# Kernel optimization log

Hardware: AMD Instinct MI355X
Metric: run time of the kernel (lower is better)

## Reference

```python
import jax, jax.numpy as jnp
import numpy as np
from jax import lax

HID = 128
NGRAPH = 64  # ligands per receptor


def _conv3d(x, w, b):
    # x: [N,C,D,H,W], w: [O,I,3,3,3], VALID padding (torch Conv3d default)
    y = lax.conv_general_dilated(x, w, (1, 1, 1), 'VALID',
                                 dimension_numbers=('NCDHW', 'OIDHW', 'NCDHW'))
    return y + b[None, :, None, None, None]


def setup_inputs() -> dict:
    key = jax.random.key(0)
    ks = jax.random.split(key, 40)
    i = iter(range(40))
    rn = lambda shape, s=1.0: jax.random.normal(ks[next(i)], shape, jnp.float32) * s
    W = 0.02
    inp = {
        'ms_feat_0': rn((4, 32, 16, 16, 16)),
        'ms_feat_1': rn((4, 64, 8, 8, 8)),
        'token_features': rn((4, 128, 256)),
        'lig_atom': rn((4, 1024, 64)),
        'lig_graph': rn((4, NGRAPH, 64)),
        'ligand_batch': jnp.sort(jax.random.randint(ks[next(i)], (1024,), 0, NGRAPH)).astype(jnp.int32),
        # token_mlp
        'W_token': rn((256, HID), W), 'b_token': jnp.zeros((HID,)),
        # pocket_mlp_list (reversed order: conv0 <- ms_feat_1 C=64, conv1 <- ms_feat_0 C=32)
        'Wc0': rn((HID, 64, 3, 3, 3), W), 'bc0': jnp.zeros((HID,)),
        'Wc1': rn((HID, 32, 3, 3, 3), W), 'bc1': jnp.zeros((HID,)),
        # pocket_mlp
        'W_pocket': rn((2 * HID, HID), W), 'b_pocket': jnp.zeros((HID,)),
        # concat layer / gate
        'W_cat': rn((3 * HID, HID), W), 'b_cat': jnp.zeros((HID,)),
        'W_gate': rn((3 * HID, HID), W), 'b_gate': jnp.zeros((HID,)),
        # ligand projections
        'W_atom': rn((64, HID), W), 'b_atom': jnp.zeros((HID,)),
        'W_graph': rn((64, HID), W), 'b_graph': jnp.zeros((HID,)),
        # energy bias mlp
        'W_bias1': rn((2 * HID, HID), W), 'b_bias1': jnp.zeros((HID,)),
        'W_bias2': rn((HID, 1), W), 'b_bias2': jnp.zeros((1,)),
        # interaction mlp + pair energy / gate
        'W_int': rn((HID, HID), W), 'b_int': jnp.zeros((HID,)),
        'W_pe': rn((HID, 1), W), 'b_pe': jnp.zeros((1,)),
        'W_pg': rn((HID, 1), W), 'b_pg': jnp.zeros((1,)),
    }
    return inp


def reference(ms_feat_0, ms_feat_1, token_features, lig_atom, lig_graph, ligand_batch,
              W_token, b_token, Wc0, bc0, Wc1, bc1, W_pocket, b_pocket,
              W_cat, b_cat, W_gate, b_gate, W_atom, b_atom, W_graph, b_graph,
              W_bias1, b_bias1, W_bias2, b_bias2, W_int, b_int,
              W_pe, b_pe, W_pg, b_pg):
    silu = jax.nn.silu
    lrelu = lambda x: jax.nn.leaky_relu(x, 0.01)

    # ---- ready_to_calculate ----
    # reversed multi-scale: [ms_feat_1, ms_feat_0]; SiLU -> Conv3d -> spatial mean
    p0 = _conv3d(silu(ms_feat_1), Wc0, bc0).mean(axis=(2, 3, 4))  # [N,HID]
    p1 = _conv3d(silu(ms_feat_0), Wc1, bc1).mean(axis=(2, 3, 4))  # [N,HID]
    pocket = silu(jnp.concatenate([p0, p1], -1)) @ W_pocket + b_pocket  # [N,HID]

    tok = silu(token_features) @ W_token + b_token                # [N,Nt,HID]
    tok_agg = jnp.concatenate([tok.sum(1), tok.mean(1)], -1)      # [N,2*HID]

    pf = jnp.concatenate([pocket, tok_agg], -1)                   # [N,3*HID]
    pf = (pf @ W_cat + b_cat) * jax.nn.sigmoid(pf @ W_gate + b_gate)  # [N,HID]

    # ---- per-image affinity (vectorized over images) ----
    atoms = lig_atom @ W_atom + b_atom                            # [N,Na,HID]
    # einsum('ik,jk->ijk') outer interaction map, batched over images
    imap = jnp.einsum('nik,njk->nijk', atoms, tok)                # [N,Na,Nt,HID]
    h = lrelu(imap @ W_int + b_int)                               # [N,Na,Nt,HID]
    pe = (h @ W_pe + b_pe) * jax.nn.sigmoid(h @ W_pg + b_pg)      # [N,Na,Nt,1]
    atom_e = pe.sum(axis=(2, 3))                                  # [N,Na]
    seg = jax.vmap(lambda v: jax.ops.segment_sum(v, ligand_batch, num_segments=NGRAPH))(atom_e)  # [N,Ng]

    gf = lig_graph @ W_graph + b_graph                            # [N,Ng,HID]
    pf_rep = jnp.broadcast_to(pf[:, None, :], gf.shape)           # [N,Ng,HID]
    z = jnp.concatenate([pf_rep, gf], -1)                         # [N,Ng,2*HID]
    bias = lrelu(z @ W_bias1 + b_bias1) @ W_bias2 + b_bias2       # [N,Ng,1]

    return seg + bias[..., 0]                                     # [N,Ng]
```

## Files before the change

### kernel.cpp

```cpp
#include <hip/hip_runtime.h>
#include <hip/hip_bf16.h>

#define NIMG 4

typedef __attribute__((ext_vector_type(8))) _Float16 half8v;
typedef __attribute__((ext_vector_type(2))) _Float16 half2v;
typedef __attribute__((ext_vector_type(4))) float float4v;
typedef __attribute__((ext_vector_type(4))) int   int4v;

__device__ __forceinline__ float sigm(float x){ return 1.f/(1.f+__expf(-x)); }
__device__ __forceinline__ float silu(float x){ return x/(1.f+__expf(-x)); }
__device__ __forceinline__ float lrelu(float x){ return fmaxf(x, 0.01f*x); }

template<int CTRL>
__device__ __forceinline__ float dpp_radd(float v){
  int s = __builtin_amdgcn_update_dpp(0, __builtin_bit_cast(int, v), CTRL, 0xF, 0xF, true);
  return v + __builtin_bit_cast(float, s);
}
__device__ __forceinline__ float row16_reduce(float v){
  v = dpp_radd<0x128>(v);
  v = dpp_radd<0x124>(v);
  v = dpp_radd<0x122>(v);
  v = dpp_radd<0x121>(v);
  return v;
}

__device__ __forceinline__ half8v scale_frag16(half8v a, const int* tpk){
  int4v ai = __builtin_bit_cast(int4v, a);
  int4v oi;
  #pragma unroll
  for(int p=0;p<4;p++){
    int r;
    asm("v_pk_mul_f16 %0, %1, %2" : "=v"(r) : "v"(ai[p]), "v"(tpk[p]));
    oi[p] = r;
  }
  return __builtin_bit_cast(half8v, oi);
}

template<int DIM, int ODIM>
__device__ void wsum_body(const float* __restrict__ x, float* __restrict__ S,
                          int vb, float* sh){
  const float* xp = x + (size_t)vb*(DIM*DIM*DIM);
  for(int p=threadIdx.x; p<DIM*DIM*DIM; p+=256) sh[p] = silu(xp[p]);
  __syncthreads();
  const int wave = threadIdx.x>>6, lane = threadIdx.x&63;
  for(int tap=wave; tap<27; tap+=4){
    const int kd=tap/9, kh=(tap/3)%3, kw=tap%3;
    const int base = kd*DIM*DIM + kh*DIM + kw;
    float ps = 0.f;
    for(int idx=lane; idx<ODIM*ODIM*ODIM; idx+=64){
      int od = idx/(ODIM*ODIM); int r = idx - od*(ODIM*ODIM);
      int oh = r/ODIM; int ow = r - oh*ODIM;
      ps += sh[base + od*DIM*DIM + oh*DIM + ow];
    }
    #pragma unroll
    for(int m=32;m>=1;m>>=1) ps += __shfl_xor(ps,m);
    if(lane==0) S[vb*27 + tap] = ps;
  }
}

__global__ __launch_bounds__(256) void k_pre(
    const float* __restrict__ tf, const float* __restrict__ Wtok,
    const float* __restrict__ btok, float* __restrict__ tok,
    const float* __restrict__ ms1, float* __restrict__ S1,
    const float* __restrict__ ms0, float* __restrict__ S0,
    const float* __restrict__ la, const float* __restrict__ Wa,
    const float* __restrict__ ba, unsigned short* __restrict__ atoms_h,
    float* __restrict__ atom_e,
    const float* __restrict__ Wint, unsigned short* __restrict__ Wt){
  __shared__ float sh[4096];
  const int b = blockIdx.x;
  const int tid = threadIdx.x;
  if(b < 512){
    const int row = b;
    sh[tid] = silu(tf[row*256 + tid]);
    __syncthreads();
    const int c = tid & 127, sg = tid >> 7;
    float acc = 0.f;
    #pragma unroll 8
    for(int q=sg*128; q<sg*128+128; q++) acc = fmaf(sh[q], Wtok[q*128+c], acc);
    if(sg==1) sh[256+c] = acc;
    __syncthreads();
    if(sg==0) tok[row*128+c] = acc + sh[256+c] + btok[c];
  } else if(b < 768){
    wsum_body<8,6>(ms1, S1, b-512, sh);
  } else if(b < 896){
    wsum_body<16,14>(ms0, S0, b-768, sh);
  } else if(b < 2944){
    const int rowb = (b-896)*2;
    if(tid < 128) sh[tid] = la[(size_t)rowb*64 + tid];
    __syncthreads();
    const int r2 = tid>>7, c = tid&127;
    const float* s = sh + r2*64;
    float acc = ba[c];
    #pragma unroll 8
    for(int k=0;k<64;k++) acc = fmaf(s[k], Wa[k*128+c], acc);
    atoms_h[(size_t)(rowb+r2)*128 + c] = __builtin_bit_cast(unsigned short, (_Float16)acc);
    if(tid<2) atom_e[rowb+tid] = 0.f;
  } else {
    const int idx = (b-2944)*256 + tid;
    const int c = idx >> 7, k = idx & 127;
    Wt[c*128 + k] = __builtin_bit_cast(unsigned short, (_Float16)(Wint[k*128 + c]));
  }
}

__global__ void k_pconv(const float* __restrict__ S1, const float* __restrict__ S0,
                        const float* __restrict__ Wc0, const float* __restrict__ bc0,
                        const float* __restrict__ Wc1, const float* __restrict__ bc1,
                        const float* __restrict__ tok, float* __restrict__ toksum,
                        float* __restrict__ pp){
  const int b = blockIdx.x;
  const int n = b >> 7, c = b & 127;
  const int tid = threadIdx.x;
  float a0 = 0.f, a1 = 0.f, ts = 0.f;
  { const float* w = Wc0 + c*1728; const float* s = S1 + n*1728;
    for(int q=tid; q<1728; q+=256) a0 = fmaf(w[q], s[q], a0); }
  { const float* w = Wc1 + c*864;  const float* s = S0 + n*864;
    for(int q=tid; q<864; q+=256)  a1 = fmaf(w[q], s[q], a1); }
  for(int j=tid; j<128; j+=256) ts = tok[(n*128+j)*128 + c];
  #pragma unroll
  for(int m=32;m>=1;m>>=1){
    a0 += __shfl_xor(a0,m); a1 += __shfl_xor(a1,m); ts += __shfl_xor(ts,m);
  }
  __shared__ float r0[4], r1[4], r2[4];
  if((tid&63)==0){ r0[tid>>6]=a0; r1[tid>>6]=a1; r2[tid>>6]=ts; }
  __syncthreads();
  if(tid==0){
    float p0 = bc0[c] + (r0[0]+r0[1]+r0[2]+r0[3])*(1.f/216.f);
    float p1 = bc1[c] + (r1[0]+r1[1]+r1[2]+r1[3])*(1.f/2744.f);
    pp[n*256 + c]       = silu(p0);
    pp[n*256 + 128 + c] = silu(p1);
    toksum[n*128 + c]   = r2[0]+r2[1]+r2[2]+r2[3];
  }
}

__global__ void k_pf2(const float* __restrict__ pp, const float* __restrict__ toksum,
                      const float* __restrict__ Wp,  const float* __restrict__ bp,
                      const float* __restrict__ Wcat, const float* __restrict__ bcat,
                      const float* __restrict__ Wgate,const float* __restrict__ bgate,
                      float* __restrict__ pf){
  __shared__ float ps[256];
  __shared__ float zz[384];
  __shared__ float part[4][128];
  __shared__ float partg[4][128];
  const int n = blockIdx.x;
  const int tid = threadIdx.x;
  const int c = tid & 127, s = tid >> 7;
  if(tid < 256) ps[tid] = pp[n*256 + tid];
  __syncthreads();
  float a = 0.f;
  for(int q=s*64; q<s*64+64; q++) a = fmaf(ps[q], Wp[q*128+c], a);
  part[s][c] = a;
  __syncthreads();
  if(s==0){
    float pk = bp[c] + part[0][c]+part[1][c]+part[2][c]+part[3][c];
    float ts = toksum[n*128+c];
    zz[c] = pk; zz[128+c] = ts; zz[256+c] = ts*(1.f/128.f);
  }
  __syncthreads();
  float a1=0.f, a2=0.f;
  for(int q=s*96; q<s*96+96; q++){
    float z = zz[q];
    a1 = fmaf(z, Wcat[q*128+c], a1);
    a2 = fmaf(z, Wgate[q*128+c], a2);
  }
  part[s][c]=a1; partg[s][c]=a2;
  __syncthreads();
  if(s==0){
    float v1 = bcat[c] +part[0][c]+part[1][c]+part[2][c]+part[3][c];
    float v2 = bgate[c]+partg[0][c]+partg[1][c]+partg[2][c]+partg[3][c];
    pf[n*128+c] = v1 * sigm(v2);
  }
}

__global__ __launch_bounds__(256,2) void k_inter(
    const unsigned short* __restrict__ atoms_h,
    const float* __restrict__ tok,
    const unsigned short* __restrict__ Wt,
    const float* __restrict__ bint,
    const float* __restrict__ Wpe, const float* __restrict__ bpe,
    const float* __restrict__ Wpg, const float* __restrict__ bpg,
    float* __restrict__ atom_e){
  __shared__ float red[8][2][2][32][2];

  const int b0 = blockIdx.x;
  const int bid = (b0 & 7)*128 + (b0 >> 3);
  const int n = bid >> 8;
  const int chunk = (bid >> 4) & 15;
  const int jg = bid & 15;
  const int tid = threadIdx.x;
  const int w = tid >> 6, lane = tid & 63;
  const int t = lane & 15, q = lane >> 4;
  const int g = w >> 1, wc = w & 1;

  const int rbase = n*1024 + chunk*64;

  half8v areg[2][4];
  { const unsigned short* ab = atoms_h + (size_t)(rbase + g*32 + t)*128 + q*8;
    #pragma unroll
    for(int fr=0;fr<2;fr++)
      #pragma unroll
      for(int ks=0;ks<4;ks++)
        areg[fr][ks] = *(const half8v*)(ab + fr*16*128 + ks*32);
  }
  half8v breg[4][4];
  { const unsigned short* wb = Wt + (size_t)(wc*64 + t)*128 + q*8;
    #pragma unroll
    for(int fc=0;fc<4;fc++)
      #pragma unroll
      for(int ks=0;ks<4;ks++)
        breg[fc][ks] = *(const half8v*)(wb + fc*16*128 + ks*32);
  }
  float bi[4], wpe[4], wpg[4];
  #pragma unroll
  for(int fc=0;fc<4;fc++){
    int cc = wc*64 + fc*16 + t;
    bi[fc]=bint[cc]; wpe[fc]=Wpe[cc]; wpg[fc]=Wpg[cc];
  }
  const float bpe0 = bpe[0], bpg0 = bpg[0];
  const float* tokn = tok + (size_t)(n*128 + jg*8)*128 + q*8;

  #pragma unroll
  for(int j=0;j<8;j++){
    int tpk[4][4];
    { const float* tr = tokn + j*128;
      #pragma unroll
      for(int ks=0;ks<4;ks++){
        float4v t0 = *(const float4v*)(tr + ks*32);
        float4v t1 = *(const float4v*)(tr + ks*32 + 4);
        tpk[ks][0] = __builtin_bit_cast(int, __builtin_amdgcn_cvt_pkrtz(t0[0],t0[1]));
        tpk[ks][1] = __builtin_bit_cast(int, __builtin_amdgcn_cvt_pkrtz(t0[2],t0[3]));
        tpk[ks][2] = __builtin_bit_cast(int, __builtin_amdgcn_cvt_pkrtz(t1[0],t1[1]));
        tpk[ks][3] = __builtin_bit_cast(int, __builtin_amdgcn_cvt_pkrtz(t1[2],t1[3]));
      }
    }
    float4v acc[2][4];
    #pragma unroll
    for(int fr=0;fr<2;fr++)
      #pragma unroll
      for(int fc=0;fc<4;fc++)
        acc[fr][fc] = (float4v){bi[fc],bi[fc],bi[fc],bi[fc]};
    #pragma unroll
    for(int ks=0;ks<4;ks++){
      half8v s0 = scale_frag16(areg[0][ks], tpk[ks]);
      half8v s1 = scale_frag16(areg[1][ks], tpk[ks]);
      #pragma unroll
      for(int fc=0;fc<4;fc++){
        acc[0][fc] = __builtin_amdgcn_mfma_f32_16x16x32_f16(s0, breg[fc][ks], acc[0][fc], 0,0,0);
        acc[1][fc] = __builtin_amdgcn_mfma_f32_16x16x32_f16(s1, breg[fc][ks], acc[1][fc], 0,0,0);
      }
    }
    #pragma unroll
    for(int fr=0;fr<2;fr++){
      #pragma unroll
      for(int r=0;r<4;r++){
        float d1=0.f, d2=0.f;
        #pragma unroll
        for(int fc=0;fc<4;fc++){
          float h = lrelu(acc[fr][fc][r]);
          d1 = fmaf(h, wpe[fc], d1);
          d2 = fmaf(h, wpg[fc], d2);
        }
        d1 = row16_reduce(d1);
        d2 = row16_reduce(d2);
        if(t==0){
          int a = fr*16 + q*4 + r;
          red[j][g][wc][a][0] = d1;
          red[j][g][wc][a][1] = d2;
        }
      }
    }
  }
  __syncthreads();
  if(tid < 64){
    const int gg = tid >> 5, a = tid & 31;
    float s_ = 0.f;
    #pragma unroll
    for(int j=0;j<8;j++){
      float d1 = red[j][gg][0][a][0] + red[j][gg][1][a][0];
      float d2 = red[j][gg][0][a][1] + red[j][gg][1][a][1];
      s_ += (d1 + bpe0) * sigm(d2 + bpg0);
    }
    atomicAdd(atom_e + rbase + tid, s_);
  }
}

__global__ __launch_bounds__(256) void k_bias_seg(
    const float* __restrict__ lg, const float* __restrict__ Wg,
    const float* __restrict__ bg, const float* __restrict__ pf,
    const float* __restrict__ W1, const float* __restrict__ b1,
    const float* __restrict__ W2, const float* __restrict__ b2,
    const float* __restrict__ atom_e, const int* __restrict__ batch,
    float* __restrict__ out){
  __shared__ float row[64];
  __shared__ float z[256];
  __shared__ float partA[128];
  __shared__ float partB[128];
  __shared__ float wred[4];
  const int b = blockIdx.x;
  const int n = b >> 6, g = b & 63;
  const int tid = threadIdx.x;
  const int c = tid & 127, s = tid >> 7;
  if(tid < 64) row[tid] = lg[b*64 + tid];
  __syncthreads();
  float gf = 0.f;
  #pragma unroll 8
  for(int k=s*32;k<s*32+32;k++) gf = fmaf(row[k], Wg[k*128+c], gf);
  if(s==1) partA[c] = gf;
  __syncthreads();
  if(s==0){ z[c] = pf[n*128+c]; z[128+c] = gf + partA[c] + bg[c]; }
  __syncthreads();
  float tacc = 0.f;
  for(int qq=s*128; qq<s*128+128; qq++) tacc = fmaf(z[qq], W1[qq*128+c], tacc);
  if(s==1) partB[c] = tacc;
  float se = 0.f;
  const float* ae = atom_e + n*1024;
  for(int i=tid;i<1024;i+=256){ float v = ae[i]; se += (batch[i]==g) ? v : 0.f; }
  __syncthreads();
  float val = se;
  if(s==0){
    float tf = lrelu(tacc + partB[c] + b1[c]);
    val += tf * W2[c];
  }
  #pragma unroll
  for(int m=32;m>=1;m>>=1) val += __shfl_xor(val,m);
  if((tid&63)==0) wred[tid>>6] = val;
  __syncthreads();
  if(tid==0) out[b] = wred[0]+wred[1]+wred[2]+wred[3] + b2[0];
}

extern "C" void kernel_launch(void* const* d_in, const int* in_sizes, int n_in,
                              void* d_out, int out_size, void* d_ws, size_t ws_size,
                              hipStream_t stream) {
  const float* ms0   = (const float*)d_in[0];
  const float* ms1   = (const float*)d_in[1];
  const float* tfeat = (const float*)d_in[2];
  const float* la    = (const float*)d_in[3];
  const float* lg    = (const float*)d_in[4];
  const int*   batch = (const int*)  d_in[5];
  const float* Wtok  = (const float*)d_in[6];
  const float* btok  = (const float*)d_in[7];
  const float* Wc0   = (const float*)d_in[8];
  const float* bc0   = (const float*)d_in[9];
  const float* Wc1   = (const float*)d_in[10];
  const float* bc1   = (const float*)d_in[11];
  const float* Wp    = (const float*)d_in[12];
  const float* bp    = (const float*)d_in[13];
  const float* Wcat  = (const float*)d_in[14];
  const float* bcat  = (const float*)d_in[15];
  const float* Wgate = (const float*)d_in[16];
  const float* bgate = (const float*)d_in[17];
  const float* Wa    = (const float*)d_in[18];
  const float* ba    = (const float*)d_in[19];
  const float* Wgr   = (const float*)d_in[20];
  const float* bgr   = (const float*)d_in[21];
  const float* W1    = (const float*)d_in[22];
  const float* b1    = (const float*)d_in[23];
  const float* W2    = (const float*)d_in[24];
  const float* b2    = (const float*)d_in[25];
  const float* Wint  = (const float*)d_in[26];
  const float* bint  = (const float*)d_in[27];
  const float* Wpe   = (const float*)d_in[28];
  const float* bpe   = (const float*)d_in[29];
  const float* Wpg   = (const float*)d_in[30];
  const float* bpg   = (const float*)d_in[31];
  float* out = (float*)d_out;

  float* ws      = (float*)d_ws;
  float* tok     = ws;
  float* S1      = ws + 65536;
  float* S0      = S1 + 6912;
  float* pp      = S0 + 3456;
  float* pf      = pp + 1024;
  float* toksum  = pf + 512;
  float* atom_e  = toksum + 512;
  unsigned short* atoms_h = (unsigned short*)(atom_e + 4096);
  unsigned short* Wt      = atoms_h + 524288;

  k_pre<<<3008, 256, 0, stream>>>(tfeat, Wtok, btok, tok,
                                  ms1, S1, ms0, S0,
                                  la, Wa, ba, atoms_h, atom_e,
                                  Wint, Wt);
  k_inter<<<1024, 256, 0, stream>>>(atoms_h, tok, Wt, bint,
                                    Wpe, bpe, Wpg, bpg, atom_e);
  k_pconv<<<NIMG*128, 256, 0, stream>>>(S1, S0, Wc0, bc0, Wc1, bc1,
                                        tok, toksum, pp);
  k_pf2<<<NIMG, 512, 0, stream>>>(pp, toksum, Wp, bp, Wcat, bcat, Wgate, bgate, pf);
  k_bias_seg<<<NIMG*64, 256, 0, stream>>>(lg, Wgr, bgr, pf, W1, b1, W2, b2,
                                          atom_e, batch, out);
}
```

Baseline: 235.3 us.

## Precompute fp16 tokens, halve k_inter rows per block, split pf2 into wide kernels

k_pre now also writes an fp16 copy of the token features, so k_inter loads half8 tokens directly and uses a plain vector multiply instead of per-iteration fp32 loads, converts and inline-asm packed multiplies. k_inter handles 32 atom rows per block instead of 64, doubling the grid to 2048 blocks, raising the occupancy hint to 3 and unrolling the token loop by 2. The single-block-per-image k_pf2 becomes two kernels with 512 blocks each, one output channel per block with wave-shuffle reductions. This adds one extra launch, and each k_inter block now reloads the full Wt fragment for half as much work.

```diff
diff --git a/kernel.cpp b/kernel.cpp
--- a/kernel.cpp
+++ b/kernel.cpp
@@ -4,9 +4,7 @@
 #define NIMG 4
 
 typedef __attribute__((ext_vector_type(8))) _Float16 half8v;
-typedef __attribute__((ext_vector_type(2))) _Float16 half2v;
 typedef __attribute__((ext_vector_type(4))) float float4v;
-typedef __attribute__((ext_vector_type(4))) int   int4v;
 
 __device__ __forceinline__ float sigm(float x){ return 1.f/(1.f+__expf(-x)); }
 __device__ __forceinline__ float silu(float x){ return x/(1.f+__expf(-x)); }
@@ -23,18 +21,6 @@
   v = dpp_radd<0x122>(v);
   v = dpp_radd<0x121>(v);
   return v;
-}
-
-__device__ __forceinline__ half8v scale_frag16(half8v a, const int* tpk){
-  int4v ai = __builtin_bit_cast(int4v, a);
-  int4v oi;
-  #pragma unroll
-  for(int p=0;p<4;p++){
-    int r;
-    asm("v_pk_mul_f16 %0, %1, %2" : "=v"(r) : "v"(ai[p]), "v"(tpk[p]));
-    oi[p] = r;
-  }
-  return __builtin_bit_cast(half8v, oi);
 }
 
 template<int DIM, int ODIM>
@@ -62,6 +48,7 @@
 __global__ __launch_bounds__(256) void k_pre(
     const float* __restrict__ tf, const float* __restrict__ Wtok,
     const float* __restrict__ btok, float* __restrict__ tok,
+    unsigned short* __restrict__ tok_h,
     const float* __restrict__ ms1, float* __restrict__ S1,
     const float* __restrict__ ms0, float* __restrict__ S0,
     const float* __restrict__ la, const float* __restrict__ Wa,
@@ -81,7 +68,11 @@
     for(int q=sg*128; q<sg*128+128; q++) acc = fmaf(sh[q], Wtok[q*128+c], acc);
     if(sg==1) sh[256+c] = acc;
     __syncthreads();
-    if(sg==0) tok[row*128+c] = acc + sh[256+c] + btok[c];
+    if(sg==0){
+      float v = acc + sh[256+c] + btok[c];
+      tok[row*128+c] = v;
+      tok_h[row*128+c] = __builtin_bit_cast(unsigned short, (_Float16)v);
+    }
   } else if(b < 768){
     wsum_body<8,6>(ms1, S1, b-512, sh);
   } else if(b < 896){
@@ -134,74 +125,81 @@
   }
 }
 
-__global__ void k_pf2(const float* __restrict__ pp, const float* __restrict__ toksum,
-                      const float* __restrict__ Wp,  const float* __restrict__ bp,
-                      const float* __restrict__ Wcat, const float* __restrict__ bcat,
-                      const float* __restrict__ Wgate,const float* __restrict__ bgate,
-                      float* __restrict__ pf){
-  __shared__ float ps[256];
+__global__ __launch_bounds__(256) void k_pock(
+    const float* __restrict__ pp, const float* __restrict__ Wp,
+    const float* __restrict__ bp, float* __restrict__ pocket){
+  const int b = blockIdx.x;
+  const int n = b >> 7, c = b & 127;
+  const int tid = threadIdx.x;
+  float a = pp[n*256 + tid] * Wp[tid*128 + c];
+  #pragma unroll
+  for(int m=32;m>=1;m>>=1) a += __shfl_xor(a,m);
+  __shared__ float r[4];
+  if((tid&63)==0) r[tid>>6] = a;
+  __syncthreads();
+  if(tid==0) pocket[n*128+c] = bp[c] + r[0]+r[1]+r[2]+r[3];
+}
+
+__global__ __launch_bounds__(256) void k_gate(
+    const float* __restrict__ pocket, const float* __restrict__ toksum,
+    const float* __restrict__ Wcat, const float* __restrict__ bcat,
+    const float* __restrict__ Wgate, const float* __restrict__ bgate,
+    float* __restrict__ pf){
   __shared__ float zz[384];
-  __shared__ float part[4][128];
-  __shared__ float partg[4][128];
-  const int n = blockIdx.x;
-  const int tid = threadIdx.x;
-  const int c = tid & 127, s = tid >> 7;
-  if(tid < 256) ps[tid] = pp[n*256 + tid];
-  __syncthreads();
-  float a = 0.f;
-  for(int q=s*64; q<s*64+64; q++) a = fmaf(ps[q], Wp[q*128+c], a);
-  part[s][c] = a;
-  __syncthreads();
-  if(s==0){
-    float pk = bp[c] + part[0][c]+part[1][c]+part[2][c]+part[3][c];
-    float ts = toksum[n*128+c];
-    zz[c] = pk; zz[128+c] = ts; zz[256+c] = ts*(1.f/128.f);
-  }
-  __syncthreads();
-  float a1=0.f, a2=0.f;
-  for(int q=s*96; q<s*96+96; q++){
+  __shared__ float r1s[4], r2s[4];
+  const int b = blockIdx.x;
+  const int n = b >> 7, c = b & 127;
+  const int tid = threadIdx.x;
+  if(tid < 128){
+    float ts = toksum[n*128 + tid];
+    zz[tid] = pocket[n*128 + tid];
+    zz[128 + tid] = ts;
+    zz[256 + tid] = ts*(1.f/128.f);
+  }
+  __syncthreads();
+  float a1 = 0.f, a2 = 0.f;
+  for(int q=tid; q<384; q+=256){
     float z = zz[q];
     a1 = fmaf(z, Wcat[q*128+c], a1);
     a2 = fmaf(z, Wgate[q*128+c], a2);
   }
-  part[s][c]=a1; partg[s][c]=a2;
-  __syncthreads();
-  if(s==0){
-    float v1 = bcat[c] +part[0][c]+part[1][c]+part[2][c]+part[3][c];
-    float v2 = bgate[c]+partg[0][c]+partg[1][c]+partg[2][c]+partg[3][c];
+  #pragma unroll
+  for(int m=32;m>=1;m>>=1){ a1 += __shfl_xor(a1,m); a2 += __shfl_xor(a2,m); }
+  if((tid&63)==0){ r1s[tid>>6]=a1; r2s[tid>>6]=a2; }
+  __syncthreads();
+  if(tid==0){
+    float v1 = bcat[c] + r1s[0]+r1s[1]+r1s[2]+r1s[3];
+    float v2 = bgate[c]+ r2s[0]+r2s[1]+r2s[2]+r2s[3];
     pf[n*128+c] = v1 * sigm(v2);
   }
 }
 
-__global__ __launch_bounds__(256,2) void k_inter(
+__global__ __launch_bounds__(256,3) void k_inter(
     const unsigned short* __restrict__ atoms_h,
-    const float* __restrict__ tok,
+    const unsigned short* __restrict__ tok_h,
     const unsigned short* __restrict__ Wt,
     const float* __restrict__ bint,
     const float* __restrict__ Wpe, const float* __restrict__ bpe,
     const float* __restrict__ Wpg, const float* __restrict__ bpg,
     float* __restrict__ atom_e){
-  __shared__ float red[8][2][2][32][2];
+  __shared__ float red[8][2][2][16][2];
 
   const int b0 = blockIdx.x;
-  const int bid = (b0 & 7)*128 + (b0 >> 3);
-  const int n = bid >> 8;
-  const int chunk = (bid >> 4) & 15;
+  const int bid = (b0 & 7)*256 + (b0 >> 3);
+  const int n = bid >> 9;
+  const int chunk = (bid >> 4) & 31;
   const int jg = bid & 15;
   const int tid = threadIdx.x;
   const int w = tid >> 6, lane = tid & 63;
   const int t = lane & 15, q = lane >> 4;
   const int g = w >> 1, wc = w & 1;
 
-  const int rbase = n*1024 + chunk*64;
-
-  half8v areg[2][4];
-  { const unsigned short* ab = atoms_h + (size_t)(rbase + g*32 + t)*128 + q*8;
-    #pragma unroll
-    for(int fr=0;fr<2;fr++)
-      #pragma unroll
-      for(int ks=0;ks<4;ks++)
-        areg[fr][ks] = *(const half8v*)(ab + fr*16*128 + ks*32);
+  const int rbase = n*1024 + chunk*32;
+
+  half8v areg[4];
+  { const unsigned short* ab = atoms_h + (size_t)(rbase + g*16 + t)*128 + q*8;
+    #pragma unroll
+    for(int ks=0;ks<4;ks++) areg[ks] = *(const half8v*)(ab + ks*32);
   }
   half8v breg[4][4];
   { const unsigned short* wb = Wt + (size_t)(wc*64 + t)*128 + q*8;
@@ -217,63 +215,44 @@
     int cc = wc*64 + fc*16 + t;
     bi[fc]=bint[cc]; wpe[fc]=Wpe[cc]; wpg[fc]=Wpg[cc];
   }
-  const float bpe0 = bpe[0], bpg0 = bpg[0];
-  const float* tokn = tok + (size_t)(n*128 + jg*8)*128 + q*8;
-
-  #pragma unroll
+  const unsigned short* tokh = tok_h + (size_t)(n*128 + jg*8)*128 + q*8;
+
+  #pragma unroll 2
   for(int j=0;j<8;j++){
-    int tpk[4][4];
-    { const float* tr = tokn + j*128;
-      #pragma unroll
-      for(int ks=0;ks<4;ks++){
-        float4v t0 = *(const float4v*)(tr + ks*32);
-        float4v t1 = *(const float4v*)(tr + ks*32 + 4);
-        tpk[ks][0] = __builtin_bit_cast(int, __builtin_amdgcn_cvt_pkrtz(t0[0],t0[1]));
-        tpk[ks][1] = __builtin_bit_cast(int, __builtin_amdgcn_cvt_pkrtz(t0[2],t0[3]));
-        tpk[ks][2] = __builtin_bit_cast(int, __builtin_amdgcn_cvt_pkrtz(t1[0],t1[1]));
-        tpk[ks][3] = __builtin_bit_cast(int, __builtin_amdgcn_cvt_pkrtz(t1[2],t1[3]));
-      }
-    }
-    float4v acc[2][4];
-    #pragma unroll
-    for(int fr=0;fr<2;fr++)
+    half8v th[4];
+    #pragma unroll
+    for(int ks=0;ks<4;ks++) th[ks] = *(const half8v*)(tokh + j*128 + ks*32);
+    float4v acc[4];
+    #pragma unroll
+    for(int fc=0;fc<4;fc++) acc[fc] = (float4v){bi[fc],bi[fc],bi[fc],bi[fc]};
+    #pragma unroll
+    for(int ks=0;ks<4;ks++){
+      half8v s = areg[ks] * th[ks];
       #pragma unroll
       for(int fc=0;fc<4;fc++)
-        acc[fr][fc] = (float4v){bi[fc],bi[fc],bi[fc],bi[fc]};
-    #pragma unroll
-    for(int ks=0;ks<4;ks++){
-      half8v s0 = scale_frag16(areg[0][ks], tpk[ks]);
-      half8v s1 = scale_frag16(areg[1][ks], tpk[ks]);
+        acc[fc] = __builtin_amdgcn_mfma_f32_16x16x32_f16(s, breg[fc][ks], acc[fc], 0,0,0);
+    }
+    #pragma unroll
+    for(int r=0;r<4;r++){
+      float d1=0.f, d2=0.f;
       #pragma unroll
       for(int fc=0;fc<4;fc++){
-        acc[0][fc] = __builtin_amdgcn_mfma_f32_16x16x32_f16(s0, breg[fc][ks], acc[0][fc], 0,0,0);
-        acc[1][fc] = __builtin_amdgcn_mfma_f32_16x16x32_f16(s1, breg[fc][ks], acc[1][fc], 0,0,0);
+        float h = lrelu(acc[fc][r]);
+        d1 = fmaf(h, wpe[fc], d1);
+        d2 = fmaf(h, wpg[fc], d2);
       }
-    }
-    #pragma unroll
-    for(int fr=0;fr<2;fr++){
-      #pragma unroll
-      for(int r=0;r<4;r++){
-        float d1=0.f, d2=0.f;
-        #pragma unroll
-        for(int fc=0;fc<4;fc++){
-          float h = lrelu(acc[fr][fc][r]);
-          d1 = fmaf(h, wpe[fc], d1);
-          d2 = fmaf(h, wpg[fc], d2);
-        }
-        d1 = row16_reduce(d1);
-        d2 = row16_reduce(d2);
-        if(t==0){
-          int a = fr*16 + q*4 + r;
-          red[j][g][wc][a][0] = d1;
-          red[j][g][wc][a][1] = d2;
-        }
+      d1 = row16_reduce(d1);
+      d2 = row16_reduce(d2);
+      if(t==0){
+        red[j][g][wc][q*4+r][0] = d1;
+        red[j][g][wc][q*4+r][1] = d2;
       }
     }
   }
   __syncthreads();
-  if(tid < 64){
-    const int gg = tid >> 5, a = tid & 31;
+  if(tid < 32){
+    const int gg = tid >> 4, a = tid & 15;
+    const float bpe0 = bpe[0], bpg0 = bpg[0];
     float s_ = 0.f;
     #pragma unroll
     for(int j=0;j<8;j++){
@@ -373,19 +352,22 @@
   float* pp      = S0 + 3456;
   float* pf      = pp + 1024;
   float* toksum  = pf + 512;
-  float* atom_e  = toksum + 512;
+  float* pocket  = toksum + 512;
+  float* atom_e  = pocket + 512;
   unsigned short* atoms_h = (unsigned short*)(atom_e + 4096);
   unsigned short* Wt      = atoms_h + 524288;
-
-  k_pre<<<3008, 256, 0, stream>>>(tfeat, Wtok, btok, tok,
+  unsigned short* tok_h   = Wt + 16384;
+
+  k_pre<<<3008, 256, 0, stream>>>(tfeat, Wtok, btok, tok, tok_h,
                                   ms1, S1, ms0, S0,
                                   la, Wa, ba, atoms_h, atom_e,
                                   Wint, Wt);
-  k_inter<<<1024, 256, 0, stream>>>(atoms_h, tok, Wt, bint,
+  k_inter<<<2048, 256, 0, stream>>>(atoms_h, tok_h, Wt, bint,
                                     Wpe, bpe, Wpg, bpg, atom_e);
   k_pconv<<<NIMG*128, 256, 0, stream>>>(S1, S0, Wc0, bc0, Wc1, bc1,
                                         tok, toksum, pp);
-  k_pf2<<<NIMG, 512, 0, stream>>>(pp, toksum, Wp, bp, Wcat, bcat, Wgate, bgate, pf);
+  k_pock<<<NIMG*128, 256, 0, stream>>>(pp, Wp, bp, pocket);
+  k_gate<<<NIMG*128, 256, 0, stream>>>(pocket, toksum, Wcat, bcat, Wgate, bgate, pf);
   k_bias_seg<<<NIMG*64, 256, 0, stream>>>(lg, Wgr, bgr, pf, W1, b1, W2, b2,
                                           atom_e, batch, out);
 }
```

New measurement: 232.9 us. No clear change (-1.0%).
